# Performance work log

Measured on AMD Instinct MI355X. Metric: run time of the kernel, lower is better.

## Reference

```python
import jax, jax.numpy as jnp
import numpy as np

B, S, D, H = 8, 1024, 768, 12
E = D // H  # head_size = 64
EPS = 1e-5


def _ln(x, g, b):
    mu = jnp.mean(x, axis=-1, keepdims=True)
    var = jnp.mean(jnp.square(x - mu), axis=-1, keepdims=True)
    return (x - mu) * jax.lax.rsqrt(var + EPS) * g + b


def setup_inputs() -> dict:
    key = jax.random.key(0)
    ks = jax.random.split(key, 16)
    w = lambda k, shape: jax.random.normal(k, shape, dtype=jnp.float32) * 0.02
    return {
        "x": jax.random.normal(ks[0], (B, S, D), dtype=jnp.float32),
        "ln1_g": jnp.ones((D,), jnp.float32),
        "ln1_b": jnp.zeros((D,), jnp.float32),
        "Wq": w(ks[1], (H, D, E)),
        "bq": w(ks[2], (H, E)),
        "Wv": w(ks[3], (H, D, E)),
        "bv": w(ks[4], (H, E)),
        "Wo": w(ks[5], (H * E, D)),
        "bo": w(ks[6], (D,)),
        "ln2_g": jnp.ones((D,), jnp.float32),
        "ln2_b": jnp.zeros((D,), jnp.float32),
        "W1": w(ks[7], (D, 4 * D)),
        "b1": w(ks[8], (4 * D,)),
        "W2": w(ks[9], (4 * D, D)),
        "b2": w(ks[10], (D,)),
    }


def reference(x, ln1_g, ln1_b, Wq, bq, Wv, bv, Wo, bo, ln2_g, ln2_b, W1, b1, W2, b2):
    d_k = x.shape[-1]
    h = _ln(x, ln1_g, ln1_b)
    # Faithful quirk: keys use the QUERY projection (k = self.query(x) in source).
    q = jnp.einsum('bsd,hde->bhse', h, Wq) + bq[None, :, None, :]
    k = q  # same projection, same input -> identical tensor
    v = jnp.einsum('bsd,hde->bhse', h, Wv) + bv[None, :, None, :]
    # Faithful quirk: scale uses full d_k, not head_size.
    scores = jnp.einsum('bhse,bhte->bhst', q, k) * (d_k ** -0.5)
    prob = jax.nn.softmax(scores, axis=-1)
    o = jnp.einsum('bhst,bhte->bhse', prob, v)  # [B,H,S,E]
    o = o.transpose(0, 2, 1, 3).reshape(x.shape[0], x.shape[1], -1)  # concat heads
    x = x + o @ Wo + bo
    h2 = _ln(x, ln2_g, ln2_b)
    mlp = jax.nn.gelu(h2 @ W1 + b1, approximate=False) @ W2 + b2
    return x + mlp
```

## Files before the change

kernel.cpp:

```cpp
#include <hip/hip_runtime.h>
#include <stdint.h>


typedef __attribute__((ext_vector_type(8))) short s8v;
typedef __attribute__((ext_vector_type(4))) float f32x4;
typedef __attribute__((ext_vector_type(4))) unsigned short us4v;

__device__ __forceinline__ unsigned short f2b(float f) {
  union { float f; unsigned u; } v; v.f = f;
  unsigned r = v.u + 0x7FFFu + ((v.u >> 16) & 1u);
  return (unsigned short)(r >> 16);
}

__device__ __forceinline__ void g2l16(const unsigned short* g, unsigned short* l) {
  __builtin_amdgcn_global_load_lds(
      (const __attribute__((address_space(1))) unsigned int*)g,
      (__attribute__((address_space(3))) unsigned int*)l, 16, 0, 0);
}

#define QSCALE 0.22816534f

__global__ __launch_bounds__(256) void repack_kernel(
    const float* __restrict__ Wq, const float* __restrict__ bq,
    const float* __restrict__ Wv, const float* __restrict__ bv,
    const float* __restrict__ Wo, const float* __restrict__ W1,
    const float* __restrict__ W2,
    unsigned short* __restrict__ Wqv_t, float* __restrict__ bias_qv,
    unsigned short* __restrict__ Wo_t, unsigned short* __restrict__ W1_t,
    unsigned short* __restrict__ W2_t)
{
  int i = blockIdx.x * 256 + threadIdx.x;
  if (i < 1536 * 768) {
    int n = i / 768, d = i % 768;
    float val;
    if (n < 768) { int h = n >> 6, e = n & 63; val = Wq[(h * 768 + d) * 64 + e] * QSCALE; }
    else { int c = n - 768; int h = c >> 6, e = c & 63; val = Wv[(h * 768 + d) * 64 + e]; }
    Wqv_t[i] = f2b(val);
  }
  if (i < 1536) bias_qv[i] = (i < 768) ? bq[i] * QSCALE : bv[i - 768];
  if (i < 768 * 768)  { int n = i / 768,  k = i % 768;  Wo_t[i] = f2b(Wo[k * 768  + n]); }
  if (i < 3072 * 768) { int n = i / 768,  k = i % 768;  W1_t[i] = f2b(W1[k * 3072 + n]); }
  if (i < 768 * 3072) { int n = i / 3072, k = i % 3072; W2_t[i] = f2b(W2[k * 768  + n]); }
}

__global__ __launch_bounds__(256) void ln_kernel(
    const float* __restrict__ x, const float* __restrict__ g,
    const float* __restrict__ b, unsigned short* __restrict__ out)
{
  __shared__ float red[4], red2[4];
  int row = blockIdx.x, t = threadIdx.x;
  const float* xr = x + (size_t)row * 768;
  float v0 = xr[t], v1 = xr[t + 256], v2 = xr[t + 512];
  float s = v0 + v1 + v2;
  #pragma unroll
  for (int m = 32; m; m >>= 1) s += __shfl_xor(s, m);
  if ((t & 63) == 0) red[t >> 6] = s;
  __syncthreads();
  float mean = (red[0] + red[1] + red[2] + red[3]) * (1.f / 768.f);
  float d0 = v0 - mean, d1 = v1 - mean, d2 = v2 - mean;
  float vs = d0 * d0 + d1 * d1 + d2 * d2;
  #pragma unroll
  for (int m = 32; m; m >>= 1) vs += __shfl_xor(vs, m);
  if ((t & 63) == 0) red2[t >> 6] = vs;
  __syncthreads();
  float var = (red2[0] + red2[1] + red2[2] + red2[3]) * (1.f / 768.f);
  float rs = rsqrtf(var + 1e-5f);
  unsigned short* o = out + (size_t)row * 768;
  o[t]       = f2b(d0 * rs * g[t]       + b[t]);
  o[t + 256] = f2b(d1 * rs * g[t + 256] + b[t + 256]);
  o[t + 512] = f2b(d2 * rs * g[t + 512] + b[t + 512]);
}

template<int NTN, int BAND>
__device__ __forceinline__ void band_map(int bid, int grid, int& m_t, int& n_t) {
  int q8 = grid >> 3;
  int mb = q8 / NTN;
  int xcd = bid & 7, idx = bid >> 3;
  constexpr int PB = 0;
  (void)PB;
  int pb = BAND * NTN;
  int band = idx / pb, r = idx % pb;
  m_t = xcd * mb + band * BAND + (r % BAND);
  n_t = r / BAND;
}

template<int EPI, int N, int K>
__global__ __launch_bounds__(512, 4) void gemm128(
    const unsigned short* __restrict__ A, const unsigned short* __restrict__ Bt,
    const float* __restrict__ bias,
    const float* resid, float* out_f32,
    unsigned short* __restrict__ out_bf,
    unsigned short* __restrict__ q_out, unsigned short* __restrict__ vt_out)
{
  __shared__ __align__(16) unsigned short As_[2][8192];
  __shared__ __align__(16) unsigned short Bs_[2][8192];
  constexpr int NTN = N >> 7;
  constexpr int NT = K >> 6;
  int m_t, n_t;
  band_map<NTN, 4>(blockIdx.x, gridDim.x, m_t, n_t);
  int m0 = m_t << 7, n0 = n_t << 7;
  int t = threadIdx.x, lane = t & 63, w = t >> 6;
  int l15 = lane & 15, lg = lane >> 4;
  int wm = (w >> 2) << 6;
  int wn = (w & 3) << 5;
  int lrow = lane >> 3;
  int lxor = ((lane & 7) ^ lrow) << 3;
  const unsigned short* Abase = A + (size_t)m0 * K;
  const unsigned short* Bbase = Bt + (size_t)n0 * K;

  auto stage = [&](int buf, int tile) {
    int k0 = tile << 6;
    #pragma unroll
    for (int j = 0; j < 2; ++j) {
      int row = j * 64 + w * 8 + lrow;
      int doff = (j * 512 + w * 64) * 8;
      g2l16(&Abase[(size_t)row * K + k0 + lxor], &As_[buf][doff]);
      g2l16(&Bbase[(size_t)row * K + k0 + lxor], &Bs_[buf][doff]);
    }
  };

  f32x4 acc[4][2] = {};
  stage(0, 0);
  asm volatile("s_waitcnt vmcnt(0)" ::: "memory");
  __builtin_amdgcn_sched_barrier(0);
  __builtin_amdgcn_s_barrier();

  int cswz = (l15 & 7) << 3;
  for (int tt = 0; tt < NT; ++tt) {
    int cur = tt & 1;
    if (tt + 1 < NT) {
      stage(cur ^ 1, tt + 1);
      asm volatile("s_waitcnt vmcnt(4)" ::: "memory");
    } else {
      asm volatile("s_waitcnt vmcnt(0)" ::: "memory");
    }
    __builtin_amdgcn_sched_barrier(0);
    __builtin_amdgcn_s_barrier();
    __builtin_amdgcn_sched_barrier(0);
    const unsigned short* Ac = &As_[cur][0];
    const unsigned short* Bc = &Bs_[cur][0];
    #pragma unroll
    for (int kk = 0; kk < 2; ++kk) {
      s8v a[4], b[2];
      int col = (kk * 32 + lg * 8) ^ cswz;
      #pragma unroll
      for (int i = 0; i < 4; ++i)
        a[i] = *(const s8v*)&Ac[(wm + i * 16 + l15) * 64 + col];
      #pragma unroll
      for (int i = 0; i < 2; ++i)
        b[i] = *(const s8v*)&Bc[(wn + i * 16 + l15) * 64 + col];
      __builtin_amdgcn_s_setprio(1);
      #pragma unroll
      for (int mi = 0; mi < 4; ++mi)
        #pragma unroll
        for (int ni = 0; ni < 2; ++ni)
          acc[mi][ni] = __builtin_amdgcn_mfma_f32_16x16x32_bf16(a[mi], b[ni], acc[mi][ni], 0, 0, 0);
      __builtin_amdgcn_s_setprio(0);
    }
    if (tt + 1 < NT) {
      __builtin_amdgcn_sched_barrier(0);
      __builtin_amdgcn_s_barrier();
      __builtin_amdgcn_sched_barrier(0);
    }
  }
  #pragma unroll
  for (int mi = 0; mi < 4; ++mi) {
    #pragma unroll
    for (int ni = 0; ni < 2; ++ni) {
      int col = n0 + wn + ni * 16 + l15;
      float bs = bias[col];
      #pragma unroll
      for (int r = 0; r < 4; ++r) {
        int row = m0 + wm + mi * 16 + lg * 4 + r;
        float v = acc[mi][ni][r] + bs;
        if (EPI == 1) {
          out_f32[(size_t)row * N + col] = resid[(size_t)row * N + col] + v;
        } else if (EPI == 2) {
          float v2 = v * v;
          float z = v * fmaf(-0.10294202f, v2, -2.302026f);
          float e; asm("v_exp_f32 %0, %1" : "=v"(e) : "v"(z));
          float rcp; asm("v_rcp_f32 %0, %1" : "=v"(rcp) : "v"(e + 1.0f));
          out_bf[(size_t)row * N + col] = f2b(v * rcp);
        } else {
          if (col < 768) {
            q_out[(size_t)row * 768 + col] = f2b(v);
          } else {
            int c = col - 768; int hh = c >> 6, e = c & 63;
            int bb = row >> 10, s = row & 1023;
            vt_out[(((size_t)(bb * 12 + hh)) * 64 + e) * 1024 + s] = f2b(v);
          }
        }
      }
    }
  }
}

template<int N, int K>
__global__ __launch_bounds__(512, 6) void gemm_n64(
    const unsigned short* __restrict__ A, const unsigned short* __restrict__ Bt,
    const float* __restrict__ bias, const float* resid, float* out_f32)
{
  __shared__ __align__(16) unsigned short As_[2][8192];
  __shared__ __align__(16) unsigned short Bs_[2][4096];
  constexpr int NTN = N >> 6;
  constexpr int NT = K >> 6;
  int m_t, n_t;
  band_map<NTN, 4>(blockIdx.x, gridDim.x, m_t, n_t);
  int m0 = m_t << 7, n0 = n_t << 6;
  int t = threadIdx.x, lane = t & 63, w = t >> 6;
  int l15 = lane & 15, lg = lane >> 4;
  int wm = (w >> 1) << 5;
  int wn = (w & 1) << 5;
  int lrow = lane >> 3;
  int lxor = ((lane & 7) ^ lrow) << 3;
  const unsigned short* Abase = A + (size_t)m0 * K;
  const unsigned short* Bbase = Bt + (size_t)n0 * K;

  auto stage = [&](int buf, int tile) {
    int k0 = tile << 6;
    #pragma unroll
    for (int j = 0; j < 2; ++j) {
      int row = j * 64 + w * 8 + lrow;
      g2l16(&Abase[(size_t)row * K + k0 + lxor], &As_[buf][(j * 512 + w * 64) * 8]);
    }
    int brow = w * 8 + lrow;
    g2l16(&Bbase[(size_t)brow * K + k0 + lxor], &Bs_[buf][w * 512]);
  };

  f32x4 acc[2][2] = {};
  stage(0, 0);
  asm volatile("s_waitcnt vmcnt(0)" ::: "memory");
  __builtin_amdgcn_sched_barrier(0);
  __builtin_amdgcn_s_barrier();

  int cswz = (l15 & 7) << 3;
  for (int tt = 0; tt < NT; ++tt) {
    int cur = tt & 1;
    if (tt + 1 < NT) {
      stage(cur ^ 1, tt + 1);
      asm volatile("s_waitcnt vmcnt(3)" ::: "memory");
    } else {
      asm volatile("s_waitcnt vmcnt(0)" ::: "memory");
    }
    __builtin_amdgcn_sched_barrier(0);
    __builtin_amdgcn_s_barrier();
    __builtin_amdgcn_sched_barrier(0);
    const unsigned short* Ac = &As_[cur][0];
    const unsigned short* Bc = &Bs_[cur][0];
    #pragma unroll
    for (int kk = 0; kk < 2; ++kk) {
      s8v a[2], b[2];
      int col = (kk * 32 + lg * 8) ^ cswz;
      #pragma unroll
      for (int i = 0; i < 2; ++i)
        a[i] = *(const s8v*)&Ac[(wm + i * 16 + l15) * 64 + col];
      #pragma unroll
      for (int i = 0; i < 2; ++i)
        b[i] = *(const s8v*)&Bc[(wn + i * 16 + l15) * 64 + col];
      __builtin_amdgcn_s_setprio(1);
      #pragma unroll
      for (int mi = 0; mi < 2; ++mi)
        #pragma unroll
        for (int ni = 0; ni < 2; ++ni)
          acc[mi][ni] = __builtin_amdgcn_mfma_f32_16x16x32_bf16(a[mi], b[ni], acc[mi][ni], 0, 0, 0);
      __builtin_amdgcn_s_setprio(0);
    }
    if (tt + 1 < NT) {
      __builtin_amdgcn_sched_barrier(0);
      __builtin_amdgcn_s_barrier();
      __builtin_amdgcn_sched_barrier(0);
    }
  }
  #pragma unroll
  for (int mi = 0; mi < 2; ++mi) {
    #pragma unroll
    for (int ni = 0; ni < 2; ++ni) {
      int col = n0 + wn + ni * 16 + l15;
      float bs = bias[col];
      #pragma unroll
      for (int r = 0; r < 4; ++r) {
        int row = m0 + wm + mi * 16 + lg * 4 + r;
        float v = acc[mi][ni][r] + bs;
        out_f32[(size_t)row * N + col] = resid[(size_t)row * N + col] + v;
      }
    }
  }
}

__global__ __launch_bounds__(256) void attn_kernel(
    const unsigned short* __restrict__ qk,
    const unsigned short* __restrict__ vt,
    unsigned short* __restrict__ o)
{
  __shared__ __align__(16) unsigned short Qs[128 * 64];
  __shared__ __align__(16) unsigned short Ks[2][64 * 64];
  __shared__ __align__(16) unsigned short Vs[2][64 * 64];
  __shared__ __align__(16) unsigned short Ps[128 * 64];
  int bid = blockIdx.x;
  int xcd = bid & 7, idx = bid >> 3;
  int bh = xcd * 12 + (idx >> 3), qt = idx & 7;
  int b = bh / 12, h = bh % 12;
  int t = threadIdx.x, lane = t & 63, w = t >> 6;
  int l15 = lane & 15, lg = lane >> 4;
  int wq0 = w << 5;
  size_t qrow0 = (size_t)b * 1024 + qt * 128;
  size_t krow0 = (size_t)b * 1024;
  size_t vbase = ((size_t)bh) * 64 * 1024;

  int srow = t >> 3;
  int scsw = ((t & 7) << 3) ^ ((srow & 7) << 3);
  const unsigned short* qsrc = &qk[(qrow0 + srow) * 768 + h * 64 + scsw];
  const unsigned short* ksrc = &qk[(krow0 + srow) * 768 + h * 64 + scsw];
  const unsigned short* vsrc = &vt[vbase + (size_t)srow * 1024 + scsw];

  #pragma unroll
  for (int j = 0; j < 4; ++j)
    g2l16(qsrc + (size_t)j * 32 * 768, &Qs[(j * 256 + w * 64) * 8]);
  #pragma unroll
  for (int j = 0; j < 2; ++j) {
    g2l16(ksrc + (size_t)j * 32 * 768, &Ks[0][(j * 256 + w * 64) * 8]);
    g2l16(vsrc + (size_t)j * 32 * 1024, &Vs[0][(j * 256 + w * 64) * 8]);
  }
  asm volatile("s_waitcnt vmcnt(0)" ::: "memory");
  __builtin_amdgcn_s_barrier();

  f32x4 oacc[4][2] = {};
  float lsum[2] = {0.f, 0.f};
  int cswz = (l15 & 7) << 3;

  for (int kt = 0; kt < 16; ++kt) {
    int buf = kt & 1;
    if (kt < 15) {
      const unsigned short* kp = ksrc + (size_t)(kt + 1) * 64 * 768;
      const unsigned short* vp = vsrc + (kt + 1) * 64;
      #pragma unroll
      for (int j = 0; j < 2; ++j) {
        g2l16(kp + (size_t)j * 32 * 768, &Ks[buf ^ 1][(j * 256 + w * 64) * 8]);
        g2l16(vp + (size_t)j * 32 * 1024, &Vs[buf ^ 1][(j * 256 + w * 64) * 8]);
      }
    }
    const unsigned short* Kb = Ks[buf];
    const unsigned short* Vb = Vs[buf];
    f32x4 st[4][2] = {};
    #pragma unroll
    for (int kk = 0; kk < 2; ++kk) {
      int col = (kk * 32 + lg * 8) ^ cswz;
      s8v a[4], bq2[2];
      #pragma unroll
      for (int i = 0; i < 4; ++i) a[i] = *(const s8v*)&Kb[(i * 16 + l15) * 64 + col];
      #pragma unroll
      for (int i = 0; i < 2; ++i) bq2[i] = *(const s8v*)&Qs[(wq0 + i * 16 + l15) * 64 + col];
      #pragma unroll
      for (int mi = 0; mi < 4; ++mi)
        #pragma unroll
        for (int ni = 0; ni < 2; ++ni)
          st[mi][ni] = __builtin_amdgcn_mfma_f32_16x16x32_bf16(a[mi], bq2[ni], st[mi][ni], 0, 0, 0);
    }
    #pragma unroll
    for (int ni = 0; ni < 2; ++ni) {
      int prow = (wq0 + ni * 16 + l15) * 64;
      #pragma unroll
      for (int mi = 0; mi < 4; ++mi) {
        float p0, p1, p2, p3;
        asm("v_exp_f32 %0, %1" : "=v"(p0) : "v"(st[mi][ni][0]));
        asm("v_exp_f32 %0, %1" : "=v"(p1) : "v"(st[mi][ni][1]));
        asm("v_exp_f32 %0, %1" : "=v"(p2) : "v"(st[mi][ni][2]));
        asm("v_exp_f32 %0, %1" : "=v"(p3) : "v"(st[mi][ni][3]));
        lsum[ni] += (p0 + p1) + (p2 + p3);
        unsigned lo, hi;
        asm("v_cvt_pk_bf16_f32 %0, %1, %2" : "=v"(lo) : "v"(p0), "v"(p1));
        asm("v_cvt_pk_bf16_f32 %0, %1, %2" : "=v"(hi) : "v"(p2), "v"(p3));
        unsigned long long pk = (unsigned long long)lo | ((unsigned long long)hi << 32);
        *(unsigned long long*)&Ps[prow + ((mi * 16 + lg * 4) ^ cswz)] = pk;
      }
    }
    #pragma unroll
    for (int kk = 0; kk < 2; ++kk) {
      int col = (kk * 32 + lg * 8) ^ cswz;
      s8v a[4], bp[2];
      #pragma unroll
      for (int i = 0; i < 4; ++i) a[i] = *(const s8v*)&Vb[(i * 16 + l15) * 64 + col];
      #pragma unroll
      for (int i = 0; i < 2; ++i) bp[i] = *(const s8v*)&Ps[(wq0 + i * 16 + l15) * 64 + col];
      #pragma unroll
      for (int ei = 0; ei < 4; ++ei)
        #pragma unroll
        for (int ni = 0; ni < 2; ++ni)
          oacc[ei][ni] = __builtin_amdgcn_mfma_f32_16x16x32_bf16(a[ei], bp[ni], oacc[ei][ni], 0, 0, 0);
    }
    asm volatile("s_waitcnt vmcnt(0)" ::: "memory");
    __builtin_amdgcn_s_barrier();
  }
  #pragma unroll
  for (int ni = 0; ni < 2; ++ni) {
    float s = lsum[ni];
    s += __shfl_xor(s, 16);
    s += __shfl_xor(s, 32);
    float inv = 1.f / s;
    int q = wq0 + ni * 16 + l15;
    size_t obase = (qrow0 + q) * 768 + h * 64;
    #pragma unroll
    for (int ei = 0; ei < 4; ++ei) {
      us4v ov;
      #pragma unroll
      for (int r = 0; r < 4; ++r) ov[r] = f2b(oacc[ei][ni][r] * inv);
      *(us4v*)&o[obase + ei * 16 + lg * 4] = ov;
    }
  }
}

extern "C" void kernel_launch(void* const* d_in, const int* in_sizes, int n_in,
                              void* d_out, int out_size, void* d_ws, size_t ws_size,
                              hipStream_t stream)
{
  const float* x     = (const float*)d_in[0];
  const float* ln1_g = (const float*)d_in[1];
  const float* ln1_b = (const float*)d_in[2];
  const float* Wq    = (const float*)d_in[3];
  const float* bq    = (const float*)d_in[4];
  const float* Wv    = (const float*)d_in[5];
  const float* bv    = (const float*)d_in[6];
  const float* Wo    = (const float*)d_in[7];
  const float* bo    = (const float*)d_in[8];
  const float* ln2_g = (const float*)d_in[9];
  const float* ln2_b = (const float*)d_in[10];
  const float* W1    = (const float*)d_in[11];
  const float* b1    = (const float*)d_in[12];
  const float* W2    = (const float*)d_in[13];
  const float* b2    = (const float*)d_in[14];
  float* out = (float*)d_out;

  char* ws = (char*)d_ws;
  size_t off = 0;
  auto alloc = [&](size_t bytes) -> void* {
    void* p = ws + off; off += (bytes + 255) & ~(size_t)255; return p;
  };
  unsigned short* Wqv_t  = (unsigned short*)alloc(1536ull * 768 * 2);
  float*          bias_qv= (float*)         alloc(1536ull * 4);
  unsigned short* Wo_t   = (unsigned short*)alloc(768ull * 768 * 2);
  unsigned short* W1_t   = (unsigned short*)alloc(3072ull * 768 * 2);
  unsigned short* W2_t   = (unsigned short*)alloc(768ull * 3072 * 2);
  unsigned short* h_bf   = (unsigned short*)alloc(8192ull * 768 * 2);
  unsigned short* q_bf   = (unsigned short*)alloc(8192ull * 768 * 2);
  unsigned short* v_t    = (unsigned short*)alloc(96ull * 64 * 1024 * 2);
  unsigned short* o_bf   = (unsigned short*)alloc(8192ull * 768 * 2);
  unsigned short* h2_bf  = (unsigned short*)alloc(8192ull * 768 * 2);
  unsigned short* m1_bf  = (unsigned short*)alloc(8192ull * 3072 * 2);

  repack_kernel<<<9216, 256, 0, stream>>>(Wq, bq, Wv, bv, Wo, W1, W2,
                                          Wqv_t, bias_qv, Wo_t, W1_t, W2_t);
  ln_kernel<<<8192, 256, 0, stream>>>(x, ln1_g, ln1_b, h_bf);
  gemm128<3, 1536, 768><<<768, 512, 0, stream>>>(h_bf, Wqv_t, bias_qv,
      nullptr, nullptr, nullptr, q_bf, v_t);
  attn_kernel<<<768, 256, 0, stream>>>(q_bf, v_t, o_bf);
  gemm128<1, 768, 768><<<384, 512, 0, stream>>>(o_bf, Wo_t, bo,
      x, out, nullptr, nullptr, nullptr);
  ln_kernel<<<8192, 256, 0, stream>>>(out, ln2_g, ln2_b, h2_bf);
  gemm128<2, 3072, 768><<<1536, 512, 0, stream>>>(h2_bf, W1_t, b1,
      nullptr, nullptr, m1_bf, nullptr, nullptr);
  gemm_n64<768, 3072><<<768, 512, 0, stream>>>(m1_bf, W2_t, b2, out, out);
}
```

Before: 267.6 us.

## Load attention K/V fragments directly from global, drop shared staging and barriers

The attention kernel no longer stages Q, K and V tiles in shared memory through async global-to-LDS copies with double buffering and block barriers. Q fragments are held in registers, and K and V fragments are loaded straight from global memory into registers each iteration. Only a per-wave P buffer stays in LDS, which shrinks shared memory use and allows a higher occupancy hint (3 blocks). The cost is that the four waves each re-read the same K/V data from global or L2 instead of sharing it, with no explicit prefetch to hide latency.

```diff
diff --git a/kernel.cpp b/kernel.cpp
--- a/kernel.cpp
+++ b/kernel.cpp
@@ -76,8 +76,6 @@
   int q8 = grid >> 3;
   int mb = q8 / NTN;
   int xcd = bid & 7, idx = bid >> 3;
-  constexpr int PB = 0;
-  (void)PB;
   int pb = BAND * NTN;
   int band = idx / pb, r = idx % pb;
   m_t = xcd * mb + band * BAND + (r % BAND);
@@ -287,15 +285,12 @@
   }
 }
 
-__global__ __launch_bounds__(256) void attn_kernel(
+__global__ __launch_bounds__(256, 3) void attn_kernel(
     const unsigned short* __restrict__ qk,
     const unsigned short* __restrict__ vt,
     unsigned short* __restrict__ o)
 {
-  __shared__ __align__(16) unsigned short Qs[128 * 64];
-  __shared__ __align__(16) unsigned short Ks[2][64 * 64];
-  __shared__ __align__(16) unsigned short Vs[2][64 * 64];
-  __shared__ __align__(16) unsigned short Ps[128 * 64];
+  __shared__ __align__(16) unsigned short Ps[4][32 * 64];
   int bid = blockIdx.x;
   int xcd = bid & 7, idx = bid >> 3;
   int bh = xcd * 12 + (idx >> 3), qt = idx & 7;
@@ -306,59 +301,39 @@
   size_t qrow0 = (size_t)b * 1024 + qt * 128;
   size_t krow0 = (size_t)b * 1024;
   size_t vbase = ((size_t)bh) * 64 * 1024;
-
-  int srow = t >> 3;
-  int scsw = ((t & 7) << 3) ^ ((srow & 7) << 3);
-  const unsigned short* qsrc = &qk[(qrow0 + srow) * 768 + h * 64 + scsw];
-  const unsigned short* ksrc = &qk[(krow0 + srow) * 768 + h * 64 + scsw];
-  const unsigned short* vsrc = &vt[vbase + (size_t)srow * 1024 + scsw];
-
-  #pragma unroll
-  for (int j = 0; j < 4; ++j)
-    g2l16(qsrc + (size_t)j * 32 * 768, &Qs[(j * 256 + w * 64) * 8]);
-  #pragma unroll
-  for (int j = 0; j < 2; ++j) {
-    g2l16(ksrc + (size_t)j * 32 * 768, &Ks[0][(j * 256 + w * 64) * 8]);
-    g2l16(vsrc + (size_t)j * 32 * 1024, &Vs[0][(j * 256 + w * 64) * 8]);
-  }
-  asm volatile("s_waitcnt vmcnt(0)" ::: "memory");
-  __builtin_amdgcn_s_barrier();
+  int cswz = (l15 & 7) << 3;
+  unsigned short* myPs = &Ps[w][0];
+
+  s8v qf[2][2];
+  #pragma unroll
+  for (int ni = 0; ni < 2; ++ni)
+    #pragma unroll
+    for (int kk = 0; kk < 2; ++kk)
+      qf[ni][kk] = *(const s8v*)&qk[(qrow0 + wq0 + ni * 16 + l15) * 768 +
+                                    h * 64 + kk * 32 + lg * 8];
 
   f32x4 oacc[4][2] = {};
   float lsum[2] = {0.f, 0.f};
-  int cswz = (l15 & 7) << 3;
 
   for (int kt = 0; kt < 16; ++kt) {
-    int buf = kt & 1;
-    if (kt < 15) {
-      const unsigned short* kp = ksrc + (size_t)(kt + 1) * 64 * 768;
-      const unsigned short* vp = vsrc + (kt + 1) * 64;
-      #pragma unroll
-      for (int j = 0; j < 2; ++j) {
-        g2l16(kp + (size_t)j * 32 * 768, &Ks[buf ^ 1][(j * 256 + w * 64) * 8]);
-        g2l16(vp + (size_t)j * 32 * 1024, &Vs[buf ^ 1][(j * 256 + w * 64) * 8]);
-      }
-    }
-    const unsigned short* Kb = Ks[buf];
-    const unsigned short* Vb = Vs[buf];
+    s8v a[4][2];
+    #pragma unroll
+    for (int i = 0; i < 4; ++i)
+      #pragma unroll
+      for (int kk = 0; kk < 2; ++kk)
+        a[i][kk] = *(const s8v*)&qk[(krow0 + kt * 64 + i * 16 + l15) * 768 +
+                                    h * 64 + kk * 32 + lg * 8];
     f32x4 st[4][2] = {};
     #pragma unroll
-    for (int kk = 0; kk < 2; ++kk) {
-      int col = (kk * 32 + lg * 8) ^ cswz;
-      s8v a[4], bq2[2];
-      #pragma unroll
-      for (int i = 0; i < 4; ++i) a[i] = *(const s8v*)&Kb[(i * 16 + l15) * 64 + col];
-      #pragma unroll
-      for (int i = 0; i < 2; ++i) bq2[i] = *(const s8v*)&Qs[(wq0 + i * 16 + l15) * 64 + col];
+    for (int kk = 0; kk < 2; ++kk)
       #pragma unroll
       for (int mi = 0; mi < 4; ++mi)
         #pragma unroll
         for (int ni = 0; ni < 2; ++ni)
-          st[mi][ni] = __builtin_amdgcn_mfma_f32_16x16x32_bf16(a[mi], bq2[ni], st[mi][ni], 0, 0, 0);
-    }
+          st[mi][ni] = __builtin_amdgcn_mfma_f32_16x16x32_bf16(a[mi][kk], qf[ni][kk], st[mi][ni], 0, 0, 0);
     #pragma unroll
     for (int ni = 0; ni < 2; ++ni) {
-      int prow = (wq0 + ni * 16 + l15) * 64;
+      int prow = (ni * 16 + l15) * 64;
       #pragma unroll
       for (int mi = 0; mi < 4; ++mi) {
         float p0, p1, p2, p3;
@@ -371,25 +346,26 @@
         asm("v_cvt_pk_bf16_f32 %0, %1, %2" : "=v"(lo) : "v"(p0), "v"(p1));
         asm("v_cvt_pk_bf16_f32 %0, %1, %2" : "=v"(hi) : "v"(p2), "v"(p3));
         unsigned long long pk = (unsigned long long)lo | ((unsigned long long)hi << 32);
-        *(unsigned long long*)&Ps[prow + ((mi * 16 + lg * 4) ^ cswz)] = pk;
+        *(unsigned long long*)&myPs[prow + ((mi * 16 + lg * 4) ^ cswz)] = pk;
       }
     }
     #pragma unroll
     for (int kk = 0; kk < 2; ++kk) {
       int col = (kk * 32 + lg * 8) ^ cswz;
-      s8v a[4], bp[2];
-      #pragma unroll
-      for (int i = 0; i < 4; ++i) a[i] = *(const s8v*)&Vb[(i * 16 + l15) * 64 + col];
-      #pragma unroll
-      for (int i = 0; i < 2; ++i) bp[i] = *(const s8v*)&Ps[(wq0 + i * 16 + l15) * 64 + col];
+      s8v vv[4], bp[2];
+      #pragma unroll
+      for (int i = 0; i < 4; ++i)
+        vv[i] = *(const s8v*)&vt[vbase + (size_t)(i * 16 + l15) * 1024 +
+                                 kt * 64 + kk * 32 + lg * 8];
+      #pragma unroll
+      for (int i = 0; i < 2; ++i)
+        bp[i] = *(const s8v*)&myPs[(i * 16 + l15) * 64 + col];
       #pragma unroll
       for (int ei = 0; ei < 4; ++ei)
         #pragma unroll
         for (int ni = 0; ni < 2; ++ni)
-          oacc[ei][ni] = __builtin_amdgcn_mfma_f32_16x16x32_bf16(a[ei], bp[ni], oacc[ei][ni], 0, 0, 0);
-    }
-    asm volatile("s_waitcnt vmcnt(0)" ::: "memory");
-    __builtin_amdgcn_s_barrier();
+          oacc[ei][ni] = __builtin_amdgcn_mfma_f32_16x16x32_bf16(vv[ei], bp[ni], oacc[ei][ni], 0, 0, 0);
+    }
   }
   #pragma unroll
   for (int ni = 0; ni < 2; ++ni) {
```

New measurement: 304.1 us. 1.14x slower.
